# Kernel optimization log

Hardware: AMD Instinct MI355X
Metric: run time of the kernel (lower is better)

Reference implementation:

```python
import jax, jax.numpy as jnp
import numpy as np

IN_FEATURES = 4096
OUT_FEATURES = 4096
LORA_R = 64
LORA_ALPHA = 16
SCALING = LORA_ALPHA / LORA_R  # 0.25


def setup_inputs() -> dict:
    key = jax.random.key(0)
    k_x, k_w, k_s, k_a, k_b = jax.random.split(key, 5)
    x = jax.random.normal(k_x, (4, 2048, IN_FEATURES), dtype=jnp.float32)
    # int8 quantized base weight in [-8, 7] as in the torch buffer init
    weight_quantized = jax.random.randint(k_w, (OUT_FEATURES, IN_FEATURES), -8, 7, dtype=jnp.int8)
    weight_scale = jax.random.normal(k_s, (1,), dtype=jnp.float32)
    lora_A = jax.random.normal(k_a, (LORA_R, IN_FEATURES), dtype=jnp.float32) * 0.01
    # torch init is zeros; use small random values so the LoRA path is exercised
    lora_B = jax.random.normal(k_b, (OUT_FEATURES, LORA_R), dtype=jnp.float32) * 0.01
    return {"x": x, "weight_quantized": weight_quantized, "weight_scale": weight_scale,
            "lora_A": lora_A, "lora_B": lora_B}


def reference(x, weight_quantized, weight_scale, lora_A, lora_B):
    # 1. dequantize base weight on the fly: [out, in]
    w_dequant = weight_quantized.astype(x.dtype) * weight_scale
    # 2. base GEMM: [B, S, in] x [in, out] -> [B, S, out]
    base = jnp.einsum('bsi,oi->bso', x, w_dequant)
    # 3. LoRA low-rank update (dropout is identity in eval mode)
    lora = jnp.einsum('bsr,or->bso', jnp.einsum('bsi,ri->bsr', x, lora_A), lora_B)
    return base + lora * SCALING
```

## Files before the change

kernel.cpp:

```cpp
#include <hip/hip_runtime.h>

#define M_TOT 8192
#define K_TOT 4096
#define N_TOT 4096
#define RANK  64
#define SCALING 0.25f

typedef __bf16 bf16x8 __attribute__((ext_vector_type(8)));
typedef float floatx4 __attribute__((ext_vector_type(4)));

static __device__ __forceinline__ unsigned short f32_to_bf16(float f) {
  unsigned int u = __float_as_uint(f);
  u += 0x7FFFu + ((u >> 16) & 1u);
  return (unsigned short)(u >> 16);
}

static __device__ __forceinline__ void async_ld16(const void* g, void* l) {
  __builtin_amdgcn_global_load_lds(
      (const __attribute__((address_space(1))) unsigned int*)g,
      (__attribute__((address_space(3))) unsigned int*)l, 16, 0, 0);
}

__global__ __launch_bounds__(256) void cvt_x_kernel(const float4* __restrict__ x,
                                                    ushort4* __restrict__ xb) {
  int i = blockIdx.x * 256 + threadIdx.x;
  float4 v = x[i];
  ushort4 o;
  o.x = f32_to_bf16(v.x);
  o.y = f32_to_bf16(v.y);
  o.z = f32_to_bf16(v.z);
  o.w = f32_to_bf16(v.w);
  xb[i] = o;
}

__global__ __launch_bounds__(256) void build_weff_kernel(
    const int* __restrict__ wq, const float* __restrict__ scale_p,
    const float* __restrict__ A, const float* __restrict__ B,
    unsigned short* __restrict__ Weff) {
  __shared__ float Bs[64][65];
  __shared__ float As[64][65];

  const int tid = threadIdx.x;
  const int o0 = blockIdx.y * 64;
  const int k0 = blockIdx.x * 64;
  const float scale = scale_p[0];

  for (int i = tid; i < 64 * 64; i += 256) {
    int o = i >> 6, r = i & 63;
    Bs[o][r] = B[(size_t)(o0 + o) * RANK + r];
  }
  for (int i = tid; i < 64 * 64; i += 256) {
    int r = i >> 6, kk = i & 63;
    As[r][kk] = A[(size_t)r * K_TOT + k0 + kk];
  }
  __syncthreads();

  const int to = tid >> 4;
  const int tk = tid & 15;
  float acc[4][4] = {};
#pragma unroll 8
  for (int r = 0; r < RANK; ++r) {
    float bv[4], av[4];
#pragma unroll
    for (int a = 0; a < 4; ++a) bv[a] = Bs[to * 4 + a][r];
#pragma unroll
    for (int b = 0; b < 4; ++b) av[b] = As[r][tk * 4 + b];
#pragma unroll
    for (int a = 0; a < 4; ++a)
#pragma unroll
      for (int b = 0; b < 4; ++b) acc[a][b] += bv[a] * av[b];
  }
#pragma unroll
  for (int a = 0; a < 4; ++a) {
    const int o = o0 + to * 4 + a;
    const size_t base = (size_t)o * K_TOT + k0 + tk * 4;
    const int4 wv = *(const int4*)(wq + base);
    ushort4 st;
    st.x = f32_to_bf16((float)wv.x * scale + SCALING * acc[a][0]);
    st.y = f32_to_bf16((float)wv.y * scale + SCALING * acc[a][1]);
    st.z = f32_to_bf16((float)wv.z * scale + SCALING * acc[a][2]);
    st.w = f32_to_bf16((float)wv.w * scale + SCALING * acc[a][3]);
    *(ushort4*)(Weff + base) = st;
  }
}

__global__ __launch_bounds__(256) void gemm_kernel(
    const unsigned short* __restrict__ Xb,
    const unsigned short* __restrict__ Wb,
    float* __restrict__ out) {
  __shared__ __align__(16) unsigned short As[2 * 128 * 32];
  __shared__ __align__(16) unsigned short Bs[2 * 128 * 32];

  const int tid = threadIdx.x;
  const int lane = tid & 63;
  const int wave = tid >> 6;
  const int wm = wave >> 1;
  const int wn = wave & 1;

  const int bM = blockIdx.y * 128;
  const int bN = blockIdx.x * 128;

  const int sRow = tid >> 2;
  const int sCol = (tid & 3) * 8;
  const unsigned short* xg0 = Xb + (size_t)(bM + sRow) * K_TOT + sCol;
  const unsigned short* xg1 = xg0 + (size_t)64 * K_TOT;
  const unsigned short* wg0 = Wb + (size_t)(bN + sRow) * K_TOT + sCol;
  const unsigned short* wg1 = wg0 + (size_t)64 * K_TOT;
  unsigned short* la00 = As + tid * 8;
  unsigned short* la01 = As + 64 * 32 + tid * 8;
  unsigned short* la10 = As + 128 * 32 + tid * 8;
  unsigned short* la11 = As + 128 * 32 + 64 * 32 + tid * 8;
  unsigned short* lb00 = Bs + tid * 8;
  unsigned short* lb01 = Bs + 64 * 32 + tid * 8;
  unsigned short* lb10 = Bs + 128 * 32 + tid * 8;
  unsigned short* lb11 = Bs + 128 * 32 + 64 * 32 + tid * 8;

  const unsigned short* pa = As + ((wm * 64) + (lane & 15)) * 32 + (lane >> 4) * 8;
  const unsigned short* pb = Bs + ((wn * 64) + (lane & 15)) * 32 + (lane >> 4) * 8;

  floatx4 acc[4][4] = {};

  for (int kt = 0; kt < K_TOT; kt += 64) {
    __syncthreads();
    async_ld16(xg0 + kt, la00);
    async_ld16(xg1 + kt, la01);
    async_ld16(xg0 + kt + 32, la10);
    async_ld16(xg1 + kt + 32, la11);
    async_ld16(wg0 + kt, lb00);
    async_ld16(wg1 + kt, lb01);
    async_ld16(wg0 + kt + 32, lb10);
    async_ld16(wg1 + kt + 32, lb11);
    __syncthreads();

#pragma unroll
    for (int ks = 0; ks < 2; ++ks) {
      const unsigned short* pak = pa + ks * 128 * 32;
      const unsigned short* pbk = pb + ks * 128 * 32;
      bf16x8 af[4], bf[4];
#pragma unroll
      for (int i = 0; i < 4; ++i) af[i] = *(const bf16x8*)(pak + i * 16 * 32);
#pragma unroll
      for (int j = 0; j < 4; ++j) bf[j] = *(const bf16x8*)(pbk + j * 16 * 32);
#pragma unroll
      for (int i = 0; i < 4; ++i)
#pragma unroll
        for (int j = 0; j < 4; ++j)
          acc[i][j] = __builtin_amdgcn_mfma_f32_16x16x32_bf16(af[i], bf[j], acc[i][j], 0, 0, 0);
    }
  }

  const int row0 = bM + wm * 64 + ((lane >> 4) << 2);
  const int col0 = bN + wn * 64 + (lane & 15);
#pragma unroll
  for (int i = 0; i < 4; ++i) {
#pragma unroll
    for (int j = 0; j < 4; ++j) {
#pragma unroll
      for (int r = 0; r < 4; ++r) {
        out[(size_t)(row0 + i * 16 + r) * N_TOT + (col0 + j * 16)] = acc[i][j][r];
      }
    }
  }
}

extern "C" void kernel_launch(void* const* d_in, const int* in_sizes, int n_in,
                              void* d_out, int out_size, void* d_ws, size_t ws_size,
                              hipStream_t stream) {
  const float* x      = (const float*)d_in[0];
  const int*   wq     = (const int*)d_in[1];
  const float* wscale = (const float*)d_in[2];
  const float* lora_A = (const float*)d_in[3];
  const float* lora_B = (const float*)d_in[4];
  float* out = (float*)d_out;

  unsigned short* xb   = (unsigned short*)d_ws;
  unsigned short* weff = (unsigned short*)((char*)d_ws + (size_t)M_TOT * K_TOT * 2);

  cvt_x_kernel<<<32768, 256, 0, stream>>>((const float4*)x, (ushort4*)xb);
  build_weff_kernel<<<dim3(K_TOT / 64, N_TOT / 64), 256, 0, stream>>>(
      wq, wscale, lora_A, lora_B, weff);
  gemm_kernel<<<dim3(N_TOT / 128, M_TOT / 128), 256, 0, stream>>>(xb, weff, out);
}
```

Before: 601.2 us.

## Rewrite bf16 GEMM as 256x256 double-buffered, swizzled, phase-interleaved MFMA kernel

Replaces the 128x128 single-stage GEMM with a 256x256 tile kernel using 512 threads, 128KB of LDS double buffering, and XOR-swizzled LDS layouts to avoid bank conflicts. Global-to-LDS loads for the next K-tile are interleaved with four MFMA phases, using explicit barriers, waitcnts and setprio. Block IDs are remapped so neighbouring blocks share L2 data. The Weff build kernel also switches to a vectorized float4 LDS read. The aim is to hide memory latency and raise MFMA utilization, at the cost of larger LDS and register use and more fragile hand synchronisation.

```diff
diff --git a/kernel.cpp b/kernel.cpp
--- a/kernel.cpp
+++ b/kernel.cpp
@@ -38,7 +38,7 @@
     const float* __restrict__ A, const float* __restrict__ B,
     unsigned short* __restrict__ Weff) {
   __shared__ float Bs[64][65];
-  __shared__ float As[64][65];
+  __shared__ __align__(16) float As[64][64];
 
   const int tid = threadIdx.x;
   const int o0 = blockIdx.y * 64;
@@ -60,11 +60,10 @@
   float acc[4][4] = {};
 #pragma unroll 8
   for (int r = 0; r < RANK; ++r) {
-    float bv[4], av[4];
+    float bv[4];
 #pragma unroll
     for (int a = 0; a < 4; ++a) bv[a] = Bs[to * 4 + a][r];
-#pragma unroll
-    for (int b = 0; b < 4; ++b) av[b] = As[r][tk * 4 + b];
+    floatx4 av = *(const floatx4*)&As[r][tk * 4];
 #pragma unroll
     for (int a = 0; a < 4; ++a)
 #pragma unroll
@@ -84,75 +83,137 @@
   }
 }
 
-__global__ __launch_bounds__(256) void gemm_kernel(
+
+template <int QM, int QN>
+static __device__ __forceinline__ void ph_mfma(floatx4 (&acc)[8][4],
+                                               const bf16x8 (&af)[4][2],
+                                               const bf16x8 (&bf)[4][2]) {
+#pragma unroll
+  for (int ii = 0; ii < 4; ++ii)
+#pragma unroll
+    for (int jj = 0; jj < 2; ++jj) {
+      floatx4 c = acc[QM * 4 + ii][QN * 2 + jj];
+      c = __builtin_amdgcn_mfma_f32_16x16x32_bf16(af[ii][0], bf[QN * 2 + jj][0], c, 0, 0, 0);
+      c = __builtin_amdgcn_mfma_f32_16x16x32_bf16(af[ii][1], bf[QN * 2 + jj][1], c, 0, 0, 0);
+      acc[QM * 4 + ii][QN * 2 + jj] = c;
+    }
+}
+
+__global__ __launch_bounds__(512, 2) void gemm_kernel(
     const unsigned short* __restrict__ Xb,
     const unsigned short* __restrict__ Wb,
     float* __restrict__ out) {
-  __shared__ __align__(16) unsigned short As[2 * 128 * 32];
-  __shared__ __align__(16) unsigned short Bs[2 * 128 * 32];
+  __shared__ __align__(16) unsigned char smem[131072];
 
   const int tid = threadIdx.x;
   const int lane = tid & 63;
   const int wave = tid >> 6;
-  const int wm = wave >> 1;
-  const int wn = wave & 1;
-
-  const int bM = blockIdx.y * 128;
-  const int bN = blockIdx.x * 128;
-
-  const int sRow = tid >> 2;
-  const int sCol = (tid & 3) * 8;
-  const unsigned short* xg0 = Xb + (size_t)(bM + sRow) * K_TOT + sCol;
-  const unsigned short* xg1 = xg0 + (size_t)64 * K_TOT;
-  const unsigned short* wg0 = Wb + (size_t)(bN + sRow) * K_TOT + sCol;
-  const unsigned short* wg1 = wg0 + (size_t)64 * K_TOT;
-  unsigned short* la00 = As + tid * 8;
-  unsigned short* la01 = As + 64 * 32 + tid * 8;
-  unsigned short* la10 = As + 128 * 32 + tid * 8;
-  unsigned short* la11 = As + 128 * 32 + 64 * 32 + tid * 8;
-  unsigned short* lb00 = Bs + tid * 8;
-  unsigned short* lb01 = Bs + 64 * 32 + tid * 8;
-  unsigned short* lb10 = Bs + 128 * 32 + tid * 8;
-  unsigned short* lb11 = Bs + 128 * 32 + 64 * 32 + tid * 8;
-
-  const unsigned short* pa = As + ((wm * 64) + (lane & 15)) * 32 + (lane >> 4) * 8;
-  const unsigned short* pb = Bs + ((wn * 64) + (lane & 15)) * 32 + (lane >> 4) * 8;
-
-  floatx4 acc[4][4] = {};
-
-  for (int kt = 0; kt < K_TOT; kt += 64) {
-    __syncthreads();
-    async_ld16(xg0 + kt, la00);
-    async_ld16(xg1 + kt, la01);
-    async_ld16(xg0 + kt + 32, la10);
-    async_ld16(xg1 + kt + 32, la11);
-    async_ld16(wg0 + kt, lb00);
-    async_ld16(wg1 + kt, lb01);
-    async_ld16(wg0 + kt + 32, lb10);
-    async_ld16(wg1 + kt + 32, lb11);
-    __syncthreads();
-
-#pragma unroll
-    for (int ks = 0; ks < 2; ++ks) {
-      const unsigned short* pak = pa + ks * 128 * 32;
-      const unsigned short* pbk = pb + ks * 128 * 32;
-      bf16x8 af[4], bf[4];
-#pragma unroll
-      for (int i = 0; i < 4; ++i) af[i] = *(const bf16x8*)(pak + i * 16 * 32);
-#pragma unroll
-      for (int j = 0; j < 4; ++j) bf[j] = *(const bf16x8*)(pbk + j * 16 * 32);
-#pragma unroll
-      for (int i = 0; i < 4; ++i)
-#pragma unroll
-        for (int j = 0; j < 4; ++j)
-          acc[i][j] = __builtin_amdgcn_mfma_f32_16x16x32_bf16(af[i], bf[j], acc[i][j], 0, 0, 0);
-    }
-  }
-
-  const int row0 = bM + wm * 64 + ((lane >> 4) << 2);
+  const int wm = wave >> 2;
+  const int wn = wave & 3;
+
+  const int bid = blockIdx.x;
+  const int swz = (bid & 7) * 64 + (bid >> 3);
+  const int bM = (swz >> 4) * 256;
+  const int bN = (swz & 15) * 256;
+
+  const int srow = tid >> 3;
+  const int scol = ((tid & 7) ^ (srow & 7)) * 8;
+  const unsigned short* xs = Xb + (size_t)(bM + srow) * K_TOT + scol;
+  const unsigned short* ws = Wb + (size_t)(bN + srow) * K_TOT + scol;
+
+  const int rb = (lane & 15) * 128;
+  const int c0 = (((lane >> 4) + 0) ^ (lane & 7)) * 16;
+  const int c1 = (((lane >> 4) + 4) ^ (lane & 7)) * 16;
+  const int aBase = wm * 16384;
+  const int bBase = 32768 + (wn >> 1) * 16384 + (wn & 1) * 8192;
+
+  floatx4 acc[8][4] = {};
+  bf16x8 af[4][2], bf[4][2];
+
+#define BAR() asm volatile("s_barrier" ::: "memory")
+#define WAIT_LGKM0() asm volatile("s_waitcnt lgkmcnt(0)" ::: "memory")
+#define WAIT_VM(N) asm volatile("s_waitcnt vmcnt(" #N ")" ::: "memory")
+#define STAGE_A(BUF, H, S, KO)                                              \
+  async_ld16(xs + (size_t)((H) * 128 + (S) * 64) * K_TOT + (KO),            \
+             smem + (BUF) * 65536 + (H) * 16384 + (S) * 8192 + tid * 16)
+#define STAGE_B(BUF, H, S, KO)                                              \
+  async_ld16(ws + (size_t)((H) * 128 + (S) * 64) * K_TOT + (KO),            \
+             smem + (BUF) * 65536 + 32768 + (H) * 16384 + (S) * 8192 + tid * 16)
+#define DSR_A(BUF, QM, II, KS)                                              \
+  af[II][KS] = *(const bf16x8*)(smem + (BUF) * 65536 + aBase +              \
+                                ((QM) * 4 + (II)) * 2048 + rb + ((KS) ? c1 : c0))
+#define DSR_B(BUF, J, KS)                                                   \
+  bf[J][KS] = *(const bf16x8*)(smem + (BUF) * 65536 + bBase +               \
+                               (J) * 2048 + rb + ((KS) ? c1 : c0))
+
+#define GROUP(BUF, KA, KB)                                                  \
+  {                                                                         \
+        \
+    DSR_A(BUF, 0, 0, 0); DSR_A(BUF, 0, 0, 1);                               \
+    DSR_A(BUF, 0, 1, 0); DSR_A(BUF, 0, 1, 1);                               \
+    DSR_A(BUF, 0, 2, 0); DSR_A(BUF, 0, 2, 1);                               \
+    DSR_A(BUF, 0, 3, 0); DSR_A(BUF, 0, 3, 1);                               \
+    DSR_B(BUF, 0, 0); DSR_B(BUF, 0, 1);                                     \
+    DSR_B(BUF, 1, 0); DSR_B(BUF, 1, 1);                                     \
+    STAGE_A((BUF) ^ 1, 0, 0, KA); STAGE_A((BUF) ^ 1, 0, 1, KA);             \
+    BAR(); WAIT_LGKM0();                                                    \
+    __builtin_amdgcn_s_setprio(1);                                          \
+    ph_mfma<0, 0>(acc, af, bf);                                             \
+    __builtin_amdgcn_s_setprio(0);                                          \
+    BAR();                                                                  \
+                 \
+    DSR_B(BUF, 2, 0); DSR_B(BUF, 2, 1);                                     \
+    DSR_B(BUF, 3, 0); DSR_B(BUF, 3, 1);                                     \
+    STAGE_A((BUF) ^ 1, 1, 0, KA); STAGE_A((BUF) ^ 1, 1, 1, KA);             \
+    BAR(); WAIT_LGKM0();                                                    \
+    __builtin_amdgcn_s_setprio(1);                                          \
+    ph_mfma<0, 1>(acc, af, bf);                                             \
+    __builtin_amdgcn_s_setprio(0);                                          \
+    BAR();                                                                  \
+     \
+    DSR_A(BUF, 1, 0, 0); DSR_A(BUF, 1, 0, 1);                               \
+    DSR_A(BUF, 1, 1, 0); DSR_A(BUF, 1, 1, 1);                               \
+    DSR_A(BUF, 1, 2, 0); DSR_A(BUF, 1, 2, 1);                               \
+    DSR_A(BUF, 1, 3, 0); DSR_A(BUF, 1, 3, 1);                               \
+    STAGE_B(BUF, 0, 0, KB); STAGE_B(BUF, 0, 1, KB);                         \
+    BAR(); WAIT_LGKM0();                                                    \
+    __builtin_amdgcn_s_setprio(1);                                          \
+    ph_mfma<1, 1>(acc, af, bf);                                             \
+    __builtin_amdgcn_s_setprio(0);                                          \
+    BAR();                                                                  \
+           \
+    STAGE_B(BUF, 1, 0, KB); STAGE_B(BUF, 1, 1, KB);                         \
+    BAR();                                                                  \
+    __builtin_amdgcn_s_setprio(1);                                          \
+    ph_mfma<1, 0>(acc, af, bf);                                             \
+    __builtin_amdgcn_s_setprio(0);                                          \
+    WAIT_VM(4);                                                             \
+    BAR();                                                                  \
+  }
+
+  STAGE_A(0, 0, 0, 0); STAGE_A(0, 0, 1, 0);
+  STAGE_A(0, 1, 0, 0); STAGE_A(0, 1, 1, 0);
+  STAGE_B(0, 0, 0, 0); STAGE_B(0, 0, 1, 0);
+  STAGE_B(0, 1, 0, 0); STAGE_B(0, 1, 1, 0);
+  STAGE_B(1, 0, 0, 64); STAGE_B(1, 0, 1, 64);
+  STAGE_B(1, 1, 0, 64); STAGE_B(1, 1, 1, 64);
+  WAIT_VM(0);
+  BAR();
+
+  for (int kt = 0; kt < 64; kt += 2) {
+    const int ka0 = ((kt + 1) & 63) * 64;
+    const int kb0 = ((kt + 2) & 63) * 64;
+    const int ka1 = ((kt + 2) & 63) * 64;
+    const int kb1 = ((kt + 3) & 63) * 64;
+    GROUP(0, ka0, kb0);
+    GROUP(1, ka1, kb1);
+  }
+  WAIT_VM(0);
+
+  const int row0 = bM + wm * 128 + ((lane >> 4) << 2);
   const int col0 = bN + wn * 64 + (lane & 15);
 #pragma unroll
-  for (int i = 0; i < 4; ++i) {
+  for (int i = 0; i < 8; ++i) {
 #pragma unroll
     for (int j = 0; j < 4; ++j) {
 #pragma unroll
@@ -161,6 +222,14 @@
       }
     }
   }
+#undef BAR
+#undef WAIT_LGKM0
+#undef WAIT_VM
+#undef STAGE_A
+#undef STAGE_B
+#undef DSR_A
+#undef DSR_B
+#undef GROUP
 }
 
 extern "C" void kernel_launch(void* const* d_in, const int* in_sizes, int n_in,
@@ -179,5 +248,5 @@
   cvt_x_kernel<<<32768, 256, 0, stream>>>((const float4*)x, (ushort4*)xb);
   build_weff_kernel<<<dim3(K_TOT / 64, N_TOT / 64), 256, 0, stream>>>(
       wq, wscale, lora_A, lora_B, weff);
-  gemm_kernel<<<dim3(N_TOT / 128, M_TOT / 128), 256, 0, stream>>>(xb, weff, out);
-}
+  gemm_kernel<<<512, 512, 0, stream>>>(xb, weff, out);
+}
```

Result: faster. 529.3 us (-12.0%).
